# Kernel optimization log

Measured on AMD Instinct MI355X. Metric: run time of the kernel, lower is better.

## Reference

```python
import jax, jax.numpy as jnp
import numpy as np

B, C, H, W = 4, 256, 64, 64
DIV = 4
D = C // DIV  # 64


def setup_inputs() -> dict:
    key = jax.random.key(0)
    ks = jax.random.split(key, 10)
    s = 0.05
    return {
        "x": jax.random.normal(ks[0], (B, C, H, W), dtype=jnp.float32),
        "wq": jax.random.normal(ks[1], (D, C), dtype=jnp.float32) * s,
        "bq": jax.random.normal(ks[2], (D,), dtype=jnp.float32) * s,
        "wk": jax.random.normal(ks[3], (D, C), dtype=jnp.float32) * s,
        "bk": jax.random.normal(ks[4], (D,), dtype=jnp.float32) * s,
        "wv": jax.random.normal(ks[5], (D, C), dtype=jnp.float32) * s,
        "bv": jax.random.normal(ks[6], (D,), dtype=jnp.float32) * s,
        "wsa": jax.random.normal(ks[7], (C, D), dtype=jnp.float32) * s,
        "bsa": jax.random.normal(ks[8], (C,), dtype=jnp.float32) * s,
        "gamma": jnp.zeros((1,), dtype=jnp.float32) + 0.5,
    }


def reference(x, wq, bq, wk, bk, wv, bv, wsa, bsa, gamma):
    b, c, h, w = x.shape
    hw = h * w
    xf = x.reshape(b, c, hw)  # [b, c, hw]
    # 1x1 convs == per-pixel linear maps
    q = jnp.einsum('dc,bcn->bdn', wq, xf) + bq[None, :, None]  # [b, d, hw]
    k = jnp.einsum('dc,bcn->bdn', wk, xf) + bk[None, :, None]
    v = jnp.einsum('dc,bcn->bdn', wv, xf) + bv[None, :, None]
    # attn[b, i, j] = softmax_j( q[:, :, i] . k[:, :, j] )
    scores = jnp.einsum('bdi,bdj->bij', q, k)  # [b, hw, hw]
    attn = jax.nn.softmax(scores, axis=-1)
    # sa = v @ attn^T : sa[b, d, i] = sum_j v[b, d, j] * attn[b, i, j]
    sa = jnp.einsum('bdj,bij->bdi', v, attn)  # [b, d, hw]
    out = jnp.einsum('cd,bdn->bcn', wsa, sa) + bsa[None, :, None]  # [b, c, hw]
    out = out.reshape(b, c, h, w)
    return gamma[0] * out + x
```

## Files before the change

kernel.cpp:

```cpp
#include <hip/hip_runtime.h>
#include <hip/hip_bf16.h>

typedef short short8 __attribute__((ext_vector_type(8)));
typedef float f32x4  __attribute__((ext_vector_type(4)));

static constexpr int NB  = 4;
static constexpr int NC  = 256;
static constexpr int NHW = 4096;
static constexpr int ND  = 64;
static constexpr int SPLIT = 8;
static constexpr int JITER = NHW / 64 / SPLIT;
static constexpr float SHIFT = 12.0f;

__device__ inline float bfbits2f(unsigned short u) {
    union { unsigned int i; float f; } x; x.i = ((unsigned int)u) << 16; return x.f;
}

__global__ __launch_bounds__(256) void wcvt_kernel(
    const float* __restrict__ wq, const float* __restrict__ wk,
    const float* __restrict__ wv, const float* __restrict__ wsa,
    __hip_bfloat16* __restrict__ wqkv_bf, __hip_bfloat16* __restrict__ wsa_bf)
{
    const int idx = blockIdx.x * 256 + threadIdx.x;
    if (idx < 192 * 256) {
        const int row = idx >> 8, col = idx & 255;
        const float* src = row < 64 ? wq : (row < 128 ? wk : wv);
        wqkv_bf[idx] = __float2bfloat16(src[(row & 63) * 256 + col]);
    } else {
        const int i = idx - 192 * 256;
        wsa_bf[i] = __float2bfloat16(wsa[i]);
    }
}

__global__ __launch_bounds__(512) void qkv_kernel(
    const float* __restrict__ x, const __hip_bfloat16* __restrict__ wqkv,
    const float* __restrict__ bq, const float* __restrict__ bk,
    const float* __restrict__ bv,
    __hip_bfloat16* __restrict__ qt, __hip_bfloat16* __restrict__ kt,
    __hip_bfloat16* __restrict__ vd)
{
    const int b  = blockIdx.x;
    const int n0 = blockIdx.y * 32;
    __shared__ __align__(16) __hip_bfloat16 xs[32][256];
    __shared__ __align__(16) __hip_bfloat16 vt_s[64][40];

    const int t  = threadIdx.x;
    const int tn = t & 31;
    const int cq = t >> 5;

    const float* xb = x + (size_t)b * NC * NHW + n0;
    #pragma unroll
    for (int kblk = 0; kblk < 4; ++kblk) {
        const int c0 = cq * 4 + kblk * 64;
        __hip_bfloat16 pk[4];
        #pragma unroll
        for (int j = 0; j < 4; ++j)
            pk[j] = __float2bfloat16(xb[(size_t)(c0 + j) * NHW + tn]);
        const int kk = (c0 >> 3) ^ (tn & 7);
        *(uint2*)&xs[tn][kk * 8 + (c0 & 7)] = *(uint2*)pk;
    }
    __syncthreads();

    const int w    = t >> 6;
    const int wm   = w >> 2;
    const int wn   = w & 3;
    const int lane = t & 63;
    const int c    = lane & 15;
    const int q    = lane >> 4;

    f32x4 acc[3];
    #pragma unroll
    for (int nt = 0; nt < 3; ++nt) acc[nt] = (f32x4){0.f, 0.f, 0.f, 0.f};

    const int row = wm * 16 + c;
    #pragma unroll
    for (int kc = 0; kc < 8; ++kc) {
        const int kk = (kc * 4 + q) ^ (row & 7);
        const short8 a = *(const short8*)&xs[row][kk * 8];
        #pragma unroll
        for (int nt = 0; nt < 3; ++nt) {
            const short8 bfr = *(const short8*)(wqkv
                + (size_t)(wn * 48 + nt * 16 + c) * 256 + kc * 32 + q * 8);
            acc[nt] = __builtin_amdgcn_mfma_f32_16x16x32_bf16(a, bfr, acc[nt], 0, 0, 0);
        }
    }

    #pragma unroll
    for (int nt = 0; nt < 3; ++nt) {
        const int j0   = wn * 48 + nt * 16;
        const int sel  = j0 >> 6;
        const int colr = (j0 & 63) + c;
        const float bias = (sel == 0 ? bq : (sel == 1 ? bk : bv))[colr];
        if (sel < 2) {
            __hip_bfloat16* dst = (sel == 0 ? qt : kt);
            #pragma unroll
            for (int r = 0; r < 4; ++r) {
                const int prow = wm * 16 + q * 4 + r;
                dst[((size_t)(b * NHW) + n0 + prow) * ND + colr] =
                    __float2bfloat16(acc[nt][r] + bias);
            }
        } else {
            #pragma unroll
            for (int r = 0; r < 4; ++r)
                vt_s[colr][wm * 16 + q * 4 + r] =
                    __float2bfloat16(acc[nt][r] + bias);
        }
    }
    __syncthreads();
    if (t < 256) {
        const int d = t >> 2, nc8 = (t & 3) * 8;
        *(short8*)(vd + ((size_t)(b * ND) + d) * NHW + n0 + nc8) =
            *(const short8*)&vt_s[d][nc8];
    }
}

__global__ __launch_bounds__(256, 4) void attn_kernel(
    const __hip_bfloat16* __restrict__ qt,
    const __hip_bfloat16* __restrict__ kt,
    const __hip_bfloat16* __restrict__ vd,
    __hip_bfloat16* __restrict__ O_part, float* __restrict__ l_part)
{
    const int b  = blockIdx.x;
    const int q0 = blockIdx.y * 128;
    const int s  = blockIdx.z;

    __shared__ __align__(16) __hip_bfloat16 ks [64][72];
    __shared__ __align__(16) __hip_bfloat16 vts[64][72];
    __shared__ __align__(16) __hip_bfloat16 ps [4][32][72];

    const int t    = threadIdx.x;
    const int w    = t >> 6;
    const int lane = t & 63;
    const int c    = lane & 15;
    const int q    = lane >> 4;

    short8 qf[2][2];
    #pragma unroll
    for (int mt = 0; mt < 2; ++mt)
        #pragma unroll
        for (int ch = 0; ch < 2; ++ch)
            qf[mt][ch] = *(const short8*)(qt
                + ((size_t)(b * NHW) + q0 + w * 32 + mt * 16 + c) * ND
                + ch * 32 + q * 8);

    f32x4 O[2][4];
    #pragma unroll
    for (int mt = 0; mt < 2; ++mt)
        #pragma unroll
        for (int dt = 0; dt < 4; ++dt)
            O[mt][dt] = (f32x4){0.f, 0.f, 0.f, 0.f};
    float lsum[2] = {0.f, 0.f};

    const int row_s = t >> 3;
    const int c8    = (t & 7) * 8;
    short8 kpre[2], vpre[2];
    {
        const int j0 = s * (NHW / SPLIT);
        kpre[0] = *(const short8*)(kt + ((size_t)(b * NHW) + j0 + row_s) * ND + c8);
        kpre[1] = *(const short8*)(kt + ((size_t)(b * NHW) + j0 + 32 + row_s) * ND + c8);
        vpre[0] = *(const short8*)(vd + ((size_t)(b * ND) + row_s) * NHW + j0 + c8);
        vpre[1] = *(const short8*)(vd + ((size_t)(b * ND) + 32 + row_s) * NHW + j0 + c8);
    }

    for (int it = 0; it < JITER; ++it) {
        __syncthreads();
        *(short8*)&ks [row_s     ][c8] = kpre[0];
        *(short8*)&ks [32 + row_s][c8] = kpre[1];
        *(short8*)&vts[row_s     ][c8] = vpre[0];
        *(short8*)&vts[32 + row_s][c8] = vpre[1];
        if (it + 1 < JITER) {
            const int j0 = s * (NHW / SPLIT) + (it + 1) * 64;
            kpre[0] = *(const short8*)(kt + ((size_t)(b * NHW) + j0 + row_s) * ND + c8);
            kpre[1] = *(const short8*)(kt + ((size_t)(b * NHW) + j0 + 32 + row_s) * ND + c8);
            vpre[0] = *(const short8*)(vd + ((size_t)(b * ND) + row_s) * NHW + j0 + c8);
            vpre[1] = *(const short8*)(vd + ((size_t)(b * ND) + 32 + row_s) * NHW + j0 + c8);
        }
        __syncthreads();

        #pragma unroll
        for (int jt = 0; jt < 4; ++jt) {
            const short8 kf0 = *(const short8*)&ks[jt * 16 + c][q * 8];
            const short8 kf1 = *(const short8*)&ks[jt * 16 + c][32 + q * 8];
            #pragma unroll
            for (int mt = 0; mt < 2; ++mt) {
                f32x4 acc = (f32x4){0.f, 0.f, 0.f, 0.f};
                acc = __builtin_amdgcn_mfma_f32_16x16x32_bf16(kf0, qf[mt][0], acc, 0, 0, 0);
                acc = __builtin_amdgcn_mfma_f32_16x16x32_bf16(kf1, qf[mt][1], acc, 0, 0, 0);
                __hip_bfloat16 pk[4];
                float ls = 0.f;
                #pragma unroll
                for (int r = 0; r < 4; ++r) {
                    const float p = __expf(acc[r] - SHIFT);
                    ls += p;
                    pk[r] = __float2bfloat16(p);
                }
                lsum[mt] += ls;
                *(uint2*)&ps[w][mt * 16 + c][jt * 16 + q * 4] = *(uint2*)pk;
            }
        }

        short8 af[2][2];
        #pragma unroll
        for (int mt = 0; mt < 2; ++mt) {
            af[mt][0] = *(const short8*)&ps[w][mt * 16 + c][q * 8];
            af[mt][1] = *(const short8*)&ps[w][mt * 16 + c][32 + q * 8];
        }
        #pragma unroll
        for (int dt = 0; dt < 4; ++dt) {
            const short8 vf0 = *(const short8*)&vts[dt * 16 + c][q * 8];
            const short8 vf1 = *(const short8*)&vts[dt * 16 + c][32 + q * 8];
            #pragma unroll
            for (int mt = 0; mt < 2; ++mt) {
                O[mt][dt] = __builtin_amdgcn_mfma_f32_16x16x32_bf16(af[mt][0], vf0, O[mt][dt], 0, 0, 0);
                O[mt][dt] = __builtin_amdgcn_mfma_f32_16x16x32_bf16(af[mt][1], vf1, O[mt][dt], 0, 0, 0);
            }
        }
    }

    const size_t sb = (size_t)(s * NB + b);
    #pragma unroll
    for (int mt = 0; mt < 2; ++mt) {
        float lv = lsum[mt];
        lv += __shfl_xor(lv, 16);
        lv += __shfl_xor(lv, 32);
        if (lane < 16)
            l_part[sb * NHW + q0 + w * 32 + mt * 16 + c] = lv;
    }
    #pragma unroll
    for (int mt = 0; mt < 2; ++mt)
        #pragma unroll
        for (int dt = 0; dt < 4; ++dt)
            #pragma unroll
            for (int r = 0; r < 4; ++r) {
                const int row = q0 + w * 32 + mt * 16 + q * 4 + r;
                O_part[(sb * NHW + row) * ND + dt * 16 + c] =
                    __float2bfloat16(O[mt][dt][r]);
            }
}

__global__ __launch_bounds__(256) void combine_kernel(
    const __hip_bfloat16* __restrict__ O_part, const float* __restrict__ l_part,
    __hip_bfloat16* __restrict__ sat)
{
    const int idx = blockIdx.x * 256 + threadIdx.x;
    const size_t bn = (size_t)(idx >> 4);
    const int d4 = (idx & 15) * 4;
    float num[4] = {0.f, 0.f, 0.f, 0.f};
    float den = 0.f;
    #pragma unroll
    for (int s = 0; s < SPLIT; ++s) {
        den += l_part[(size_t)s * NB * NHW + bn];
        const unsigned short* op = (const unsigned short*)(O_part
            + ((size_t)s * NB * NHW + bn) * ND + d4);
        ushort4 u = *(const ushort4*)op;
        num[0] += bfbits2f(u.x); num[1] += bfbits2f(u.y);
        num[2] += bfbits2f(u.z); num[3] += bfbits2f(u.w);
    }
    const float inv = 1.f / den;
    __hip_bfloat16 o[4];
    #pragma unroll
    for (int j = 0; j < 4; ++j) o[j] = __float2bfloat16(num[j] * inv);
    *(uint2*)(sat + bn * ND + d4) = *(uint2*)o;
}

__global__ __launch_bounds__(512) void out_kernel(
    const __hip_bfloat16* __restrict__ sat,
    const __hip_bfloat16* __restrict__ wsa_bf,
    const float* __restrict__ bsa, const float* __restrict__ g,
    const float* __restrict__ x, float* __restrict__ out)
{
    const int b  = blockIdx.x;
    const int n0 = blockIdx.y * 32;
    const int t  = threadIdx.x;
    const int w  = t >> 6;
    const int lane = t & 63;
    const int c  = lane & 15;
    const int q  = lane >> 4;

    short8 bf[2][2];
    #pragma unroll
    for (int nt = 0; nt < 2; ++nt)
        #pragma unroll
        for (int ch = 0; ch < 2; ++ch)
            bf[nt][ch] = *(const short8*)(sat
                + ((size_t)(b * NHW) + n0 + nt * 16 + c) * ND + ch * 32 + q * 8);

    short8 af[2][2];
    #pragma unroll
    for (int mt = 0; mt < 2; ++mt)
        #pragma unroll
        for (int ch = 0; ch < 2; ++ch)
            af[mt][ch] = *(const short8*)(wsa_bf
                + ((size_t)(w * 32 + mt * 16 + c)) * ND + ch * 32 + q * 8);

    f32x4 acc[2][2];
    #pragma unroll
    for (int mt = 0; mt < 2; ++mt)
        #pragma unroll
        for (int nt = 0; nt < 2; ++nt) {
            f32x4 a = (f32x4){0.f, 0.f, 0.f, 0.f};
            a = __builtin_amdgcn_mfma_f32_16x16x32_bf16(af[mt][0], bf[nt][0], a, 0, 0, 0);
            a = __builtin_amdgcn_mfma_f32_16x16x32_bf16(af[mt][1], bf[nt][1], a, 0, 0, 0);
            acc[mt][nt] = a;
        }

    const float gamma = g[0];
    #pragma unroll
    for (int mt = 0; mt < 2; ++mt) {
        float biasr[4];
        #pragma unroll
        for (int r = 0; r < 4; ++r)
            biasr[r] = bsa[w * 32 + mt * 16 + q * 4 + r];
        #pragma unroll
        for (int nt = 0; nt < 2; ++nt)
            #pragma unroll
            for (int r = 0; r < 4; ++r) {
                const int crow = w * 32 + mt * 16 + q * 4 + r;
                const size_t oi = ((size_t)(b * NC) + crow) * NHW + n0 + nt * 16 + c;
                out[oi] = gamma * (acc[mt][nt][r] + biasr[r]) + x[oi];
            }
    }
}

extern "C" void kernel_launch(void* const* d_in, const int* in_sizes, int n_in,
                              void* d_out, int out_size, void* d_ws, size_t ws_size,
                              hipStream_t stream)
{
    const float* x     = (const float*)d_in[0];
    const float* wq    = (const float*)d_in[1];
    const float* bq    = (const float*)d_in[2];
    const float* wk    = (const float*)d_in[3];
    const float* bk    = (const float*)d_in[4];
    const float* wv    = (const float*)d_in[5];
    const float* bv    = (const float*)d_in[6];
    const float* wsa   = (const float*)d_in[7];
    const float* bsa   = (const float*)d_in[8];
    const float* gamma = (const float*)d_in[9];
    float* out = (float*)d_out;

    char* p = (char*)d_ws;
    __hip_bfloat16* wqkv_bf = (__hip_bfloat16*)p; p += (size_t)128 << 10;
    __hip_bfloat16* wsa_bf  = (__hip_bfloat16*)p; p += (size_t)128 << 10;
    __hip_bfloat16* qt = (__hip_bfloat16*)p; p += (size_t)2 << 20;
    __hip_bfloat16* kt = (__hip_bfloat16*)p; p += (size_t)2 << 20;
    __hip_bfloat16* vd = (__hip_bfloat16*)p; p += (size_t)2 << 20;
    __hip_bfloat16* O_part = (__hip_bfloat16*)p; p += (size_t)16 << 20;
    float* l_part = (float*)p; p += (size_t)1 << 20;
    __hip_bfloat16* sat = (__hip_bfloat16*)p; p += (size_t)2 << 20;

    wcvt_kernel<<<dim3(256), 256, 0, stream>>>(wq, wk, wv, wsa, wqkv_bf, wsa_bf);
    qkv_kernel<<<dim3(NB, NHW / 32), 512, 0, stream>>>(
        x, wqkv_bf, bq, bk, bv, qt, kt, vd);
    attn_kernel<<<dim3(NB, NHW / 128, SPLIT), 256, 0, stream>>>(
        qt, kt, vd, O_part, l_part);
    combine_kernel<<<dim3(NB * NHW * 16 / 256), 256, 0, stream>>>(
        O_part, l_part, sat);
    out_kernel<<<dim3(NB, NHW / 32), 512, 0, stream>>>(
        sat, wsa_bf, bsa, gamma, x, out);
}
```

Before: 137.7 us.

## Fuse split combine into output projection, use exp2 and stage O stores via LDS

Removes the separate combine kernel by having the output-projection kernel reduce the split-K partial results and normalise them into shared memory before the MFMA. Folds log2(e) into the Q weights and bias so softmax can use exp2f, and folds gamma into the converted output weights. Partial O stores in the attention kernel are staged through shared memory for 16-byte coalesced writes. This saves one launch and the sat round trip through global memory, and trades that for reduction work moved into out_kernel and an extra LDS pass in attention.

```diff
diff --git a/kernel.cpp b/kernel.cpp
--- a/kernel.cpp
+++ b/kernel.cpp
@@ -10,7 +10,8 @@
 static constexpr int ND  = 64;
 static constexpr int SPLIT = 8;
 static constexpr int JITER = NHW / 64 / SPLIT;
-static constexpr float SHIFT = 12.0f;
+static constexpr float LOG2E  = 1.44269504f;
+static constexpr float SHIFT2 = 12.0f * 1.44269504f;
 
 __device__ inline float bfbits2f(unsigned short u) {
     union { unsigned int i; float f; } x; x.i = ((unsigned int)u) << 16; return x.f;
@@ -19,16 +20,19 @@
 __global__ __launch_bounds__(256) void wcvt_kernel(
     const float* __restrict__ wq, const float* __restrict__ wk,
     const float* __restrict__ wv, const float* __restrict__ wsa,
-    __hip_bfloat16* __restrict__ wqkv_bf, __hip_bfloat16* __restrict__ wsa_bf)
+    const float* __restrict__ g,
+    __hip_bfloat16* __restrict__ wqkv_bf, __hip_bfloat16* __restrict__ wsa_g)
 {
     const int idx = blockIdx.x * 256 + threadIdx.x;
     if (idx < 192 * 256) {
         const int row = idx >> 8, col = idx & 255;
         const float* src = row < 64 ? wq : (row < 128 ? wk : wv);
-        wqkv_bf[idx] = __float2bfloat16(src[(row & 63) * 256 + col]);
+        float v = src[(row & 63) * 256 + col];
+        if (row < 64) v *= LOG2E;
+        wqkv_bf[idx] = __float2bfloat16(v);
     } else {
         const int i = idx - 192 * 256;
-        wsa_bf[i] = __float2bfloat16(wsa[i]);
+        wsa_g[i] = __float2bfloat16(wsa[i] * g[0]);
     }
 }
 
@@ -90,7 +94,8 @@
         const int j0   = wn * 48 + nt * 16;
         const int sel  = j0 >> 6;
         const int colr = (j0 & 63) + c;
-        const float bias = (sel == 0 ? bq : (sel == 1 ? bk : bv))[colr];
+        const float bias = (sel == 0 ? bq[colr] * LOG2E
+                                     : (sel == 1 ? bk : bv)[colr]);
         if (sel < 2) {
             __hip_bfloat16* dst = (sel == 0 ? qt : kt);
             #pragma unroll
@@ -190,7 +195,7 @@
                 float ls = 0.f;
                 #pragma unroll
                 for (int r = 0; r < 4; ++r) {
-                    const float p = __expf(acc[r] - SHIFT);
+                    const float p = exp2f(acc[r] - SHIFT2);
                     ls += p;
                     pk[r] = __float2bfloat16(p);
                 }
@@ -231,66 +236,70 @@
         #pragma unroll
         for (int dt = 0; dt < 4; ++dt)
             #pragma unroll
-            for (int r = 0; r < 4; ++r) {
-                const int row = q0 + w * 32 + mt * 16 + q * 4 + r;
-                O_part[(sb * NHW + row) * ND + dt * 16 + c] =
+            for (int r = 0; r < 4; ++r)
+                ps[w][mt * 16 + q * 4 + r][dt * 16 + c] =
                     __float2bfloat16(O[mt][dt][r]);
-            }
-}
-
-__global__ __launch_bounds__(256) void combine_kernel(
+    const int lrow = lane >> 3;
+    const int ld0  = (lane & 7) * 8;
+    #pragma unroll
+    for (int rr = 0; rr < 4; ++rr) {
+        const int row = rr * 8 + lrow;
+        const short8 ov = *(const short8*)&ps[w][row][ld0];
+        *(short8*)(O_part + (sb * NHW + q0 + w * 32 + row) * ND + ld0) = ov;
+    }
+}
+
+__global__ __launch_bounds__(512) void out_kernel(
     const __hip_bfloat16* __restrict__ O_part, const float* __restrict__ l_part,
-    __hip_bfloat16* __restrict__ sat)
-{
-    const int idx = blockIdx.x * 256 + threadIdx.x;
-    const size_t bn = (size_t)(idx >> 4);
-    const int d4 = (idx & 15) * 4;
-    float num[4] = {0.f, 0.f, 0.f, 0.f};
-    float den = 0.f;
-    #pragma unroll
-    for (int s = 0; s < SPLIT; ++s) {
-        den += l_part[(size_t)s * NB * NHW + bn];
-        const unsigned short* op = (const unsigned short*)(O_part
-            + ((size_t)s * NB * NHW + bn) * ND + d4);
-        ushort4 u = *(const ushort4*)op;
-        num[0] += bfbits2f(u.x); num[1] += bfbits2f(u.y);
-        num[2] += bfbits2f(u.z); num[3] += bfbits2f(u.w);
-    }
-    const float inv = 1.f / den;
-    __hip_bfloat16 o[4];
-    #pragma unroll
-    for (int j = 0; j < 4; ++j) o[j] = __float2bfloat16(num[j] * inv);
-    *(uint2*)(sat + bn * ND + d4) = *(uint2*)o;
-}
-
-__global__ __launch_bounds__(512) void out_kernel(
-    const __hip_bfloat16* __restrict__ sat,
-    const __hip_bfloat16* __restrict__ wsa_bf,
+    const __hip_bfloat16* __restrict__ wsa_g,
     const float* __restrict__ bsa, const float* __restrict__ g,
     const float* __restrict__ x, float* __restrict__ out)
 {
     const int b  = blockIdx.x;
     const int n0 = blockIdx.y * 32;
+    __shared__ __align__(16) __hip_bfloat16 sat_s[32][72];
     const int t  = threadIdx.x;
-    const int w  = t >> 6;
+
+    {
+        const int pix = t >> 4;
+        const int d4  = (t & 15) * 4;
+        const size_t bn = (size_t)(b * NHW) + n0 + pix;
+        float num[4] = {0.f, 0.f, 0.f, 0.f};
+        float den = 0.f;
+        #pragma unroll
+        for (int s = 0; s < SPLIT; ++s) {
+            den += l_part[(size_t)s * NB * NHW + bn];
+            const ushort4 u = *(const ushort4*)(O_part
+                + ((size_t)s * NB * NHW + bn) * ND + d4);
+            num[0] += bfbits2f(u.x); num[1] += bfbits2f(u.y);
+            num[2] += bfbits2f(u.z); num[3] += bfbits2f(u.w);
+        }
+        const float inv = 1.f / den;
+        __hip_bfloat16 o[4];
+        #pragma unroll
+        for (int j = 0; j < 4; ++j) o[j] = __float2bfloat16(num[j] * inv);
+        *(uint2*)&sat_s[pix][d4] = *(uint2*)o;
+    }
+    __syncthreads();
+
+    const int w    = t >> 6;
     const int lane = t & 63;
-    const int c  = lane & 15;
-    const int q  = lane >> 4;
-
-    short8 bf[2][2];
+    const int c    = lane & 15;
+    const int q    = lane >> 4;
+
+    short8 bfrag[2][2];
     #pragma unroll
     for (int nt = 0; nt < 2; ++nt)
         #pragma unroll
         for (int ch = 0; ch < 2; ++ch)
-            bf[nt][ch] = *(const short8*)(sat
-                + ((size_t)(b * NHW) + n0 + nt * 16 + c) * ND + ch * 32 + q * 8);
+            bfrag[nt][ch] = *(const short8*)&sat_s[nt * 16 + c][ch * 32 + q * 8];
 
     short8 af[2][2];
     #pragma unroll
     for (int mt = 0; mt < 2; ++mt)
         #pragma unroll
         for (int ch = 0; ch < 2; ++ch)
-            af[mt][ch] = *(const short8*)(wsa_bf
+            af[mt][ch] = *(const short8*)(wsa_g
                 + ((size_t)(w * 32 + mt * 16 + c)) * ND + ch * 32 + q * 8);
 
     f32x4 acc[2][2];
@@ -299,25 +308,25 @@
         #pragma unroll
         for (int nt = 0; nt < 2; ++nt) {
             f32x4 a = (f32x4){0.f, 0.f, 0.f, 0.f};
-            a = __builtin_amdgcn_mfma_f32_16x16x32_bf16(af[mt][0], bf[nt][0], a, 0, 0, 0);
-            a = __builtin_amdgcn_mfma_f32_16x16x32_bf16(af[mt][1], bf[nt][1], a, 0, 0, 0);
+            a = __builtin_amdgcn_mfma_f32_16x16x32_bf16(af[mt][0], bfrag[nt][0], a, 0, 0, 0);
+            a = __builtin_amdgcn_mfma_f32_16x16x32_bf16(af[mt][1], bfrag[nt][1], a, 0, 0, 0);
             acc[mt][nt] = a;
         }
 
     const float gamma = g[0];
     #pragma unroll
     for (int mt = 0; mt < 2; ++mt) {
-        float biasr[4];
+        float gbias[4];
         #pragma unroll
         for (int r = 0; r < 4; ++r)
-            biasr[r] = bsa[w * 32 + mt * 16 + q * 4 + r];
+            gbias[r] = gamma * bsa[w * 32 + mt * 16 + q * 4 + r];
         #pragma unroll
         for (int nt = 0; nt < 2; ++nt)
             #pragma unroll
             for (int r = 0; r < 4; ++r) {
                 const int crow = w * 32 + mt * 16 + q * 4 + r;
                 const size_t oi = ((size_t)(b * NC) + crow) * NHW + n0 + nt * 16 + c;
-                out[oi] = gamma * (acc[mt][nt][r] + biasr[r]) + x[oi];
+                out[oi] = acc[mt][nt][r] + gbias[r] + x[oi];
             }
     }
 }
@@ -340,21 +349,19 @@
 
     char* p = (char*)d_ws;
     __hip_bfloat16* wqkv_bf = (__hip_bfloat16*)p; p += (size_t)128 << 10;
-    __hip_bfloat16* wsa_bf  = (__hip_bfloat16*)p; p += (size_t)128 << 10;
+    __hip_bfloat16* wsa_g   = (__hip_bfloat16*)p; p += (size_t)128 << 10;
     __hip_bfloat16* qt = (__hip_bfloat16*)p; p += (size_t)2 << 20;
     __hip_bfloat16* kt = (__hip_bfloat16*)p; p += (size_t)2 << 20;
     __hip_bfloat16* vd = (__hip_bfloat16*)p; p += (size_t)2 << 20;
-    __hip_bfloat16* O_part = (__hip_bfloat16*)p; p += (size_t)16 << 20;
+    __hip_bfloat16* O_part = (__hip_bfloat16*)p; p += (size_t)18 << 20;
     float* l_part = (float*)p; p += (size_t)1 << 20;
-    __hip_bfloat16* sat = (__hip_bfloat16*)p; p += (size_t)2 << 20;
-
-    wcvt_kernel<<<dim3(256), 256, 0, stream>>>(wq, wk, wv, wsa, wqkv_bf, wsa_bf);
+
+    wcvt_kernel<<<dim3(256), 256, 0, stream>>>(
+        wq, wk, wv, wsa, gamma, wqkv_bf, wsa_g);
     qkv_kernel<<<dim3(NB, NHW / 32), 512, 0, stream>>>(
         x, wqkv_bf, bq, bk, bv, qt, kt, vd);
     attn_kernel<<<dim3(NB, NHW / 128, SPLIT), 256, 0, stream>>>(
         qt, kt, vd, O_part, l_part);
-    combine_kernel<<<dim3(NB * NHW * 16 / 256), 256, 0, stream>>>(
-        O_part, l_part, sat);
     out_kernel<<<dim3(NB, NHW / 32), 512, 0, stream>>>(
-        sat, wsa_bf, bsa, gamma, x, out);
-}
+        O_part, l_part, wsa_g, bsa, gamma, x, out);
+}
```

Result: slower. 140.7 us (+2.2%).
